# Optimization experiments

Measured on AMD Instinct MI355X. Metric: run time of the kernel, lower is better.

Reference implementation:

```python
import jax, jax.numpy as jnp
import numpy as np

B, TV, TH, F, H, D = 16, 128, 64, 512, 512, 256


def setup_inputs() -> dict:
    key = jax.random.key(0)
    ks = jax.random.split(key, 6)
    return {
        "v": jax.random.normal(ks[0], (B, TV, F), dtype=jnp.float32),
        "h": jax.random.normal(ks[1], (B, TH, H), dtype=jnp.float32),
        "W": jax.random.normal(ks[2], (F, D), dtype=jnp.float32) * 0.05,
        "U": jax.random.normal(ks[3], (H, D), dtype=jnp.float32) * 0.05,
        "b": jax.random.normal(ks[4], (D,), dtype=jnp.float32) * 0.05,
        "w": jax.random.normal(ks[5], (D, 1), dtype=jnp.float32) * 0.05,
    }


def reference(v, h, W, U, b, w):
    # v: [B, Tv, F] video features; h: [B, Th, H] decoder hidden states
    Wv = jnp.einsum("btf,fd->btd", v, W)      # [B, Tv, D]
    Uh = jnp.einsum("bsh,hd->bsd", h, U)      # [B, Th, D]
    # Broadcast add -> [B, Th, Tv, D], tanh nonlinearity (additive attention)
    f = jnp.tanh(Uh[:, :, None, :] + Wv[:, None, :, :] + b)
    q = jnp.einsum("bstd,d->bst", f, w[:, 0])  # scores [B, Th, Tv]
    beta = jax.nn.softmax(q, axis=-1)           # softmax over Tv (axis -2 of q[..., None])
    u = jnp.einsum("bst,btf->bsf", beta, v)    # context [B, Th, F]
    return u
```

## Files before the change

### kernel.cpp

```cpp
#include <hip/hip_runtime.h>
#include <hip/hip_bf16.h>

#define BB 16
#define TV 128
#define TH 64
#define FF 512
#define HH 512
#define DD 256

#define LOG2E2 2.8853900817779268f

typedef __attribute__((ext_vector_type(8))) short bf16x8;
typedef __attribute__((ext_vector_type(4))) float f32x4;

__device__ __forceinline__ float fast_exp2(float x) {
#if __has_builtin(__builtin_amdgcn_exp2f)
  return __builtin_amdgcn_exp2f(x);
#else
  return __expf(x * 0.6931471805599453f);
#endif
}
__device__ __forceinline__ float fast_rcp(float x) {
#if __has_builtin(__builtin_amdgcn_rcpf)
  return __builtin_amdgcn_rcpf(x);
#else
  return 1.0f / x;
#endif
}
__device__ __forceinline__ unsigned short f2bf(float x) {
  union { float f; unsigned u; } a; a.f = x;
  unsigned r = a.u + 0x7fffu + ((a.u >> 16) & 1u);
  return (unsigned short)(r >> 16);
}

#define NT_V 262144
#define NT_H 131072
#define NT_W 32768
__global__ __launch_bounds__(256) void convert_kernel(
    const float* __restrict__ v, const float* __restrict__ h,
    const float* __restrict__ W, const float* __restrict__ U,
    unsigned short* __restrict__ vb, unsigned short* __restrict__ hb,
    unsigned short* __restrict__ WT, unsigned short* __restrict__ UT) {
  int task = blockIdx.x * 256 + threadIdx.x;
  if (task < NT_V) {
    float4 x = ((const float4*)v)[task];
    ushort4 o = make_ushort4(f2bf(x.x), f2bf(x.y), f2bf(x.z), f2bf(x.w));
    *(ushort4*)&vb[(size_t)task * 4] = o;
  } else if (task < NT_V + NT_H) {
    int t2 = task - NT_V;
    float4 x = ((const float4*)h)[t2];
    ushort4 o = make_ushort4(f2bf(x.x), f2bf(x.y), f2bf(x.z), f2bf(x.w));
    *(ushort4*)&hb[(size_t)t2 * 4] = o;
  } else {
    int t2 = task - NT_V - NT_H;
    const float* S;
    unsigned short* Dt;
    if (t2 < NT_W) { S = W; Dt = WT; } else { S = U; Dt = UT; t2 -= NT_W; }
    int n = t2 & 255, k4 = t2 >> 8;
    float a0 = S[(k4 * 4 + 0) * 256 + n];
    float a1 = S[(k4 * 4 + 1) * 256 + n];
    float a2 = S[(k4 * 4 + 2) * 256 + n];
    float a3 = S[(k4 * 4 + 3) * 256 + n];
    ushort4 o = make_ushort4(f2bf(a0), f2bf(a1), f2bf(a2), f2bf(a3));
    *(ushort4*)&Dt[(size_t)n * 512 + k4 * 4] = o;
  }
}

__global__ __launch_bounds__(128) void mfma_gemm_kernel(
    const unsigned short* __restrict__ Av, const unsigned short* __restrict__ Ah,
    const unsigned short* __restrict__ WT, const unsigned short* __restrict__ UT,
    const float* __restrict__ bias, float* __restrict__ Wv2T,
    float* __restrict__ Uh2) {
  const int bid = blockIdx.x;
  const unsigned short* A;
  const unsigned short* BT;
  int mt, nt;
  bool is_wv;
  if (bid < 256) {
    A = Av; BT = WT; is_wv = true;
    mt = bid >> 3; nt = bid & 7;
  } else {
    const int b2 = bid - 256;
    A = Ah; BT = UT; is_wv = false;
    mt = b2 >> 3; nt = b2 & 7;
  }
  const int wv   = threadIdx.x >> 6;
  const int lane = threadIdx.x & 63;
  const int m0   = mt * 64 + wv * 32;
  const int n0   = nt * 32;
  const int r16  = lane & 15;
  const int quad = lane >> 4;

  const unsigned short* a0p = A + (size_t)(m0 + r16) * 512 + quad * 8;
  const unsigned short* a1p = a0p + 16 * 512;
  const unsigned short* b0p = BT + (size_t)(n0 + r16) * 512 + quad * 8;
  const unsigned short* b1p = b0p + 16 * 512;

  f32x4 acc00 = {0.f, 0.f, 0.f, 0.f};
  f32x4 acc01 = {0.f, 0.f, 0.f, 0.f};
  f32x4 acc10 = {0.f, 0.f, 0.f, 0.f};
  f32x4 acc11 = {0.f, 0.f, 0.f, 0.f};

#pragma unroll
  for (int kc = 0; kc < 16; kc++) {
    bf16x8 a0 = *(const bf16x8*)(a0p + kc * 32);
    bf16x8 a1 = *(const bf16x8*)(a1p + kc * 32);
    bf16x8 b0 = *(const bf16x8*)(b0p + kc * 32);
    bf16x8 b1 = *(const bf16x8*)(b1p + kc * 32);
    acc00 = __builtin_amdgcn_mfma_f32_16x16x32_bf16(a0, b0, acc00, 0, 0, 0);
    acc01 = __builtin_amdgcn_mfma_f32_16x16x32_bf16(a0, b1, acc01, 0, 0, 0);
    acc10 = __builtin_amdgcn_mfma_f32_16x16x32_bf16(a1, b0, acc10, 0, 0, 0);
    acc11 = __builtin_amdgcn_mfma_f32_16x16x32_bf16(a1, b1, acc11, 0, 0, 0);
  }

  if (is_wv) {
    const int bb   = m0 >> 7;
    const int tb   = (m0 & 127) + quad * 4;
    float* Wb = Wv2T + (size_t)bb * 32768;
#pragma unroll
    for (int r = 0; r < 4; r++) {
      Wb[(size_t)(n0 + r16) * 128 + tb + r]        = acc00[r] * LOG2E2;
      Wb[(size_t)(n0 + 16 + r16) * 128 + tb + r]   = acc01[r] * LOG2E2;
      Wb[(size_t)(n0 + r16) * 128 + tb + 16 + r]   = acc10[r] * LOG2E2;
      Wb[(size_t)(n0 + 16 + r16) * 128 + tb + 16 + r] = acc11[r] * LOG2E2;
    }
  } else {
    const float bj0 = bias[n0 + r16];
    const float bj1 = bias[n0 + 16 + r16];
#pragma unroll
    for (int r = 0; r < 4; r++) {
      const int row0 = m0 + quad * 4 + r;
      Uh2[(size_t)row0 * 256 + n0 + r16]             = (acc00[r] + bj0) * LOG2E2;
      Uh2[(size_t)row0 * 256 + n0 + 16 + r16]        = (acc01[r] + bj1) * LOG2E2;
      Uh2[(size_t)(row0 + 16) * 256 + n0 + r16]      = (acc10[r] + bj0) * LOG2E2;
      Uh2[(size_t)(row0 + 16) * 256 + n0 + 16 + r16] = (acc11[r] + bj1) * LOG2E2;
    }
  }
}

__global__ __launch_bounds__(1024) void attn_fused_kernel(
    const float* __restrict__ Wv2T, const float* __restrict__ Uh2,
    const float* __restrict__ wg, const float* __restrict__ v,
    float* __restrict__ u) {
  __shared__ float UhS[4 * 256];
  __shared__ float wS[256];
  __shared__ float pS[4 * 1024];
  __shared__ float bS[4 * 128];
  __shared__ float mW[8];
  __shared__ float sW[8];

  const int tid = threadIdx.x;
  const int b   = blockIdx.x >> 4;
  const int sg  = blockIdx.x & 15;
  const int s0  = sg * 4;

  if (tid < 256) {
    const int row = tid >> 6, q4 = (tid & 63) << 2;
    *(float4*)&UhS[row * 256 + q4] =
        *(const float4*)&Uh2[(size_t)(b * 64 + s0 + row) * 256 + q4];
  } else if (tid < 320) {
    const int q4 = (tid - 256) << 2;
    *(float4*)&wS[q4] = *(const float4*)&wg[q4];
  }
  __syncthreads();

  {
    const int t4 = tid & 31;
    const int dg = (tid >> 5) & 7;
    const int s  = tid >> 8;
    const float* wvb = Wv2T + (size_t)b * 32768 + (size_t)dg * 32 * 128 + t4 * 4;
    const float* uhp = &UhS[s * 256 + dg * 32];
    const float* wp  = &wS[dg * 32];
    float4 acc = {0.f, 0.f, 0.f, 0.f};
#pragma unroll 8
    for (int j = 0; j < 32; j++) {
      float4 a  = *(const float4*)(wvb + j * 128);
      float uh = uhp[j];
      float ww = wp[j];
      acc.x = fmaf(ww, fast_rcp(fast_exp2(a.x + uh) + 1.0f), acc.x);
      acc.y = fmaf(ww, fast_rcp(fast_exp2(a.y + uh) + 1.0f), acc.y);
      acc.z = fmaf(ww, fast_rcp(fast_exp2(a.z + uh) + 1.0f), acc.z);
      acc.w = fmaf(ww, fast_rcp(fast_exp2(a.w + uh) + 1.0f), acc.w);
    }
    *(float4*)&pS[s * 1024 + dg * 128 + t4 * 4] = acc;
  }
  __syncthreads();

  float qv = 0.0f, ev = 0.0f;
  const int wvid = tid >> 6, lane = tid & 63;
  if (tid < 512) {
    const int s_l = tid >> 7, t = tid & 127;
    float ssum = 0.0f;
#pragma unroll
    for (int dg = 0; dg < 8; dg++) ssum += pS[s_l * 1024 + dg * 128 + t];
    qv = ssum * (-LOG2E2);
    float m = qv;
#pragma unroll
    for (int off = 32; off > 0; off >>= 1) m = fmaxf(m, __shfl_xor(m, off, 64));
    if (lane == 0) mW[wvid] = m;
  }
  __syncthreads();
  if (tid < 512) {
    float m = fmaxf(mW[wvid], mW[wvid ^ 1]);
    ev = fast_exp2(qv - m);
    float ssum = ev;
#pragma unroll
    for (int off = 32; off > 0; off >>= 1) ssum += __shfl_xor(ssum, off, 64);
    if (lane == 0) sW[wvid] = ssum;
  }
  __syncthreads();
  if (tid < 512) {
    const int s_l = tid >> 7, t = tid & 127;
    bS[s_l * 128 + t] = ev * fast_rcp(sW[wvid] + sW[wvid ^ 1]);
  }
  __syncthreads();

  const float* vb2 = v + (size_t)b * TV * FF;
  const int f  = tid & 511;
  const int sh = tid >> 9;
  float a0 = 0.f, a1 = 0.f;
#pragma unroll 4
  for (int tg = 0; tg < 128; tg += 4) {
    float4 b0 = *(const float4*)&bS[(sh * 2 + 0) * 128 + tg];
    float4 b1 = *(const float4*)&bS[(sh * 2 + 1) * 128 + tg];
    float v0 = vb2[(tg + 0) * 512 + f];
    float v1 = vb2[(tg + 1) * 512 + f];
    float v2 = vb2[(tg + 2) * 512 + f];
    float v3 = vb2[(tg + 3) * 512 + f];
    a0 = fmaf(b0.x, v0, a0); a0 = fmaf(b0.y, v1, a0);
    a0 = fmaf(b0.z, v2, a0); a0 = fmaf(b0.w, v3, a0);
    a1 = fmaf(b1.x, v0, a1); a1 = fmaf(b1.y, v1, a1);
    a1 = fmaf(b1.z, v2, a1); a1 = fmaf(b1.w, v3, a1);
  }
  float* urow = u + (size_t)(b * 64 + s0 + sh * 2) * 512;
  urow[0 * 512 + f] = a0;
  urow[1 * 512 + f] = a1;
}

extern "C" void kernel_launch(void* const* d_in, const int* in_sizes, int n_in,
                              void* d_out, int out_size, void* d_ws, size_t ws_size,
                              hipStream_t stream) {
  const float* v  = (const float*)d_in[0];
  const float* h  = (const float*)d_in[1];
  const float* W  = (const float*)d_in[2];
  const float* U  = (const float*)d_in[3];
  const float* bb = (const float*)d_in[4];
  const float* w  = (const float*)d_in[5];
  float* u = (float*)d_out;

  float* Wv2T = (float*)d_ws;
  float* Uh2  = Wv2T + (size_t)2048 * 256;
  unsigned short* vb16 = (unsigned short*)(Uh2 + (size_t)1024 * 256);
  unsigned short* hb16 = vb16 + (size_t)2048 * 512;
  unsigned short* WT   = hb16 + (size_t)1024 * 512;
  unsigned short* UT   = WT + (size_t)256 * 512;

  convert_kernel<<<1792, 256, 0, stream>>>(v, h, W, U, vb16, hb16, WT, UT);
  mfma_gemm_kernel<<<384, 128, 0, stream>>>(vb16, hb16, WT, UT, bb, Wv2T, Uh2);
  attn_fused_kernel<<<256, 1024, 0, stream>>>(Wv2T, Uh2, w, v, u);
}
```

Baseline: 92.87 us.

## Rebalance GEMM and attention grids, read bf16 video features in context sum

The GEMM now uses 256-thread blocks covering 128 rows each, so it launches half as many blocks, and the Wv transposed output is written as float4 stores instead of scalar ones. The attention kernel drops to 512 threads handling 2 query rows per block and runs 512 blocks, which gives more blocks for the same work. It also reads the bf16 copy of v in the final weighted sum, halving the bytes read there. The risks are that each v element is now reloaded by twice as many blocks, and that using bf16 v in the context sum adds rounding error to the output.

```diff
diff --git a/kernel.cpp b/kernel.cpp
--- a/kernel.cpp
+++ b/kernel.cpp
@@ -31,6 +31,10 @@
   union { float f; unsigned u; } a; a.f = x;
   unsigned r = a.u + 0x7fffu + ((a.u >> 16) & 1u);
   return (unsigned short)(r >> 16);
+}
+__device__ __forceinline__ float bf2f(unsigned short x) {
+  union { unsigned u; float f; } a; a.u = ((unsigned)x) << 16;
+  return a.f;
 }
 
 #define NT_V 262144
@@ -66,7 +70,7 @@
   }
 }
 
-__global__ __launch_bounds__(128) void mfma_gemm_kernel(
+__global__ __launch_bounds__(256) void mfma_gemm_kernel(
     const unsigned short* __restrict__ Av, const unsigned short* __restrict__ Ah,
     const unsigned short* __restrict__ WT, const unsigned short* __restrict__ UT,
     const float* __restrict__ bias, float* __restrict__ Wv2T,
@@ -76,17 +80,17 @@
   const unsigned short* BT;
   int mt, nt;
   bool is_wv;
-  if (bid < 256) {
+  if (bid < 128) {
     A = Av; BT = WT; is_wv = true;
     mt = bid >> 3; nt = bid & 7;
   } else {
-    const int b2 = bid - 256;
+    const int b2 = bid - 128;
     A = Ah; BT = UT; is_wv = false;
     mt = b2 >> 3; nt = b2 & 7;
   }
   const int wv   = threadIdx.x >> 6;
   const int lane = threadIdx.x & 63;
-  const int m0   = mt * 64 + wv * 32;
+  const int m0   = mt * 128 + wv * 32;
   const int n0   = nt * 32;
   const int r16  = lane & 15;
   const int quad = lane >> 4;
@@ -101,7 +105,7 @@
   f32x4 acc10 = {0.f, 0.f, 0.f, 0.f};
   f32x4 acc11 = {0.f, 0.f, 0.f, 0.f};
 
-#pragma unroll
+#pragma unroll 4
   for (int kc = 0; kc < 16; kc++) {
     bf16x8 a0 = *(const bf16x8*)(a0p + kc * 32);
     bf16x8 a1 = *(const bf16x8*)(a1p + kc * 32);
@@ -114,16 +118,20 @@
   }
 
   if (is_wv) {
-    const int bb   = m0 >> 7;
-    const int tb   = (m0 & 127) + quad * 4;
-    float* Wb = Wv2T + (size_t)bb * 32768;
+    const int tb = (m0 & 127) + quad * 4;
+    float* Wb = Wv2T + (size_t)mt * 32768;
+    float4 s00, s01, s10, s11;
 #pragma unroll
     for (int r = 0; r < 4; r++) {
-      Wb[(size_t)(n0 + r16) * 128 + tb + r]        = acc00[r] * LOG2E2;
-      Wb[(size_t)(n0 + 16 + r16) * 128 + tb + r]   = acc01[r] * LOG2E2;
-      Wb[(size_t)(n0 + r16) * 128 + tb + 16 + r]   = acc10[r] * LOG2E2;
-      Wb[(size_t)(n0 + 16 + r16) * 128 + tb + 16 + r] = acc11[r] * LOG2E2;
+      (&s00.x)[r] = acc00[r] * LOG2E2;
+      (&s01.x)[r] = acc01[r] * LOG2E2;
+      (&s10.x)[r] = acc10[r] * LOG2E2;
+      (&s11.x)[r] = acc11[r] * LOG2E2;
     }
+    *(float4*)&Wb[(size_t)(n0 + r16) * 128 + tb]           = s00;
+    *(float4*)&Wb[(size_t)(n0 + r16) * 128 + tb + 16]      = s10;
+    *(float4*)&Wb[(size_t)(n0 + 16 + r16) * 128 + tb]      = s01;
+    *(float4*)&Wb[(size_t)(n0 + 16 + r16) * 128 + tb + 16] = s11;
   } else {
     const float bj0 = bias[n0 + r16];
     const float bj1 = bias[n0 + 16 + r16];
@@ -138,28 +146,28 @@
   }
 }
 
-__global__ __launch_bounds__(1024) void attn_fused_kernel(
+__global__ __launch_bounds__(512) void attn_fused_kernel(
     const float* __restrict__ Wv2T, const float* __restrict__ Uh2,
-    const float* __restrict__ wg, const float* __restrict__ v,
+    const float* __restrict__ wg, const unsigned short* __restrict__ vb16,
     float* __restrict__ u) {
-  __shared__ float UhS[4 * 256];
+  __shared__ float UhS[2 * 256];
   __shared__ float wS[256];
-  __shared__ float pS[4 * 1024];
-  __shared__ float bS[4 * 128];
-  __shared__ float mW[8];
-  __shared__ float sW[8];
+  __shared__ float pS[8 * 2 * 128];
+  __shared__ float bS[2 * 128];
+  __shared__ float mW[4];
+  __shared__ float sW[4];
 
   const int tid = threadIdx.x;
-  const int b   = blockIdx.x >> 4;
-  const int sg  = blockIdx.x & 15;
-  const int s0  = sg * 4;
-
-  if (tid < 256) {
+  const int b   = blockIdx.x >> 5;
+  const int sg  = blockIdx.x & 31;
+  const int s0  = sg * 2;
+
+  if (tid < 128) {
     const int row = tid >> 6, q4 = (tid & 63) << 2;
     *(float4*)&UhS[row * 256 + q4] =
         *(const float4*)&Uh2[(size_t)(b * 64 + s0 + row) * 256 + q4];
-  } else if (tid < 320) {
-    const int q4 = (tid - 256) << 2;
+  } else if (tid < 192) {
+    const int q4 = (tid - 128) << 2;
     *(float4*)&wS[q4] = *(const float4*)&wg[q4];
   }
   __syncthreads();
@@ -169,30 +177,35 @@
     const int dg = (tid >> 5) & 7;
     const int s  = tid >> 8;
     const float* wvb = Wv2T + (size_t)b * 32768 + (size_t)dg * 32 * 128 + t4 * 4;
-    const float* uhp = &UhS[s * 256 + dg * 32];
-    const float* wp  = &wS[dg * 32];
+    const float4* uhq = (const float4*)&UhS[s * 256 + dg * 32];
+    const float4* wq  = (const float4*)&wS[dg * 32];
     float4 acc = {0.f, 0.f, 0.f, 0.f};
-#pragma unroll 8
-    for (int j = 0; j < 32; j++) {
-      float4 a  = *(const float4*)(wvb + j * 128);
-      float uh = uhp[j];
-      float ww = wp[j];
-      acc.x = fmaf(ww, fast_rcp(fast_exp2(a.x + uh) + 1.0f), acc.x);
-      acc.y = fmaf(ww, fast_rcp(fast_exp2(a.y + uh) + 1.0f), acc.y);
-      acc.z = fmaf(ww, fast_rcp(fast_exp2(a.z + uh) + 1.0f), acc.z);
-      acc.w = fmaf(ww, fast_rcp(fast_exp2(a.w + uh) + 1.0f), acc.w);
+#pragma unroll
+    for (int jq = 0; jq < 8; jq++) {
+      float4 uh4 = uhq[jq];
+      float4 w4  = wq[jq];
+#pragma unroll
+      for (int jj = 0; jj < 4; jj++) {
+        float4 a  = *(const float4*)(wvb + (jq * 4 + jj) * 128);
+        float uh = (&uh4.x)[jj];
+        float ww = (&w4.x)[jj];
+        acc.x = fmaf(ww, fast_rcp(fast_exp2(a.x + uh) + 1.0f), acc.x);
+        acc.y = fmaf(ww, fast_rcp(fast_exp2(a.y + uh) + 1.0f), acc.y);
+        acc.z = fmaf(ww, fast_rcp(fast_exp2(a.z + uh) + 1.0f), acc.z);
+        acc.w = fmaf(ww, fast_rcp(fast_exp2(a.w + uh) + 1.0f), acc.w);
+      }
     }
-    *(float4*)&pS[s * 1024 + dg * 128 + t4 * 4] = acc;
+    *(float4*)&pS[(dg * 2 + s) * 128 + t4 * 4] = acc;
   }
   __syncthreads();
 
   float qv = 0.0f, ev = 0.0f;
   const int wvid = tid >> 6, lane = tid & 63;
-  if (tid < 512) {
+  if (tid < 256) {
     const int s_l = tid >> 7, t = tid & 127;
     float ssum = 0.0f;
 #pragma unroll
-    for (int dg = 0; dg < 8; dg++) ssum += pS[s_l * 1024 + dg * 128 + t];
+    for (int dg = 0; dg < 8; dg++) ssum += pS[(dg * 2 + s_l) * 128 + t];
     qv = ssum * (-LOG2E2);
     float m = qv;
 #pragma unroll
@@ -200,7 +213,7 @@
     if (lane == 0) mW[wvid] = m;
   }
   __syncthreads();
-  if (tid < 512) {
+  if (tid < 256) {
     float m = fmaxf(mW[wvid], mW[wvid ^ 1]);
     ev = fast_exp2(qv - m);
     float ssum = ev;
@@ -209,30 +222,29 @@
     if (lane == 0) sW[wvid] = ssum;
   }
   __syncthreads();
-  if (tid < 512) {
+  if (tid < 256) {
     const int s_l = tid >> 7, t = tid & 127;
     bS[s_l * 128 + t] = ev * fast_rcp(sW[wvid] + sW[wvid ^ 1]);
   }
   __syncthreads();
 
-  const float* vb2 = v + (size_t)b * TV * FF;
-  const int f  = tid & 511;
-  const int sh = tid >> 9;
+  const unsigned short* vb2 = vb16 + (size_t)b * TV * FF;
+  const int f = tid;
   float a0 = 0.f, a1 = 0.f;
 #pragma unroll 4
   for (int tg = 0; tg < 128; tg += 4) {
-    float4 b0 = *(const float4*)&bS[(sh * 2 + 0) * 128 + tg];
-    float4 b1 = *(const float4*)&bS[(sh * 2 + 1) * 128 + tg];
-    float v0 = vb2[(tg + 0) * 512 + f];
-    float v1 = vb2[(tg + 1) * 512 + f];
-    float v2 = vb2[(tg + 2) * 512 + f];
-    float v3 = vb2[(tg + 3) * 512 + f];
+    float4 b0 = *(const float4*)&bS[0 * 128 + tg];
+    float4 b1 = *(const float4*)&bS[1 * 128 + tg];
+    float v0 = bf2f(vb2[(tg + 0) * 512 + f]);
+    float v1 = bf2f(vb2[(tg + 1) * 512 + f]);
+    float v2 = bf2f(vb2[(tg + 2) * 512 + f]);
+    float v3 = bf2f(vb2[(tg + 3) * 512 + f]);
     a0 = fmaf(b0.x, v0, a0); a0 = fmaf(b0.y, v1, a0);
     a0 = fmaf(b0.z, v2, a0); a0 = fmaf(b0.w, v3, a0);
     a1 = fmaf(b1.x, v0, a1); a1 = fmaf(b1.y, v1, a1);
     a1 = fmaf(b1.z, v2, a1); a1 = fmaf(b1.w, v3, a1);
   }
-  float* urow = u + (size_t)(b * 64 + s0 + sh * 2) * 512;
+  float* urow = u + (size_t)(b * 64 + s0) * 512;
   urow[0 * 512 + f] = a0;
   urow[1 * 512 + f] = a1;
 }
@@ -256,6 +268,6 @@
   unsigned short* UT   = WT + (size_t)256 * 512;
 
   convert_kernel<<<1792, 256, 0, stream>>>(v, h, W, U, vb16, hb16, WT, UT);
-  mfma_gemm_kernel<<<384, 128, 0, stream>>>(vb16, hb16, WT, UT, bb, Wv2T, Uh2);
-  attn_fused_kernel<<<256, 1024, 0, stream>>>(Wv2T, Uh2, w, v, u);
-}
+  mfma_gemm_kernel<<<192, 256, 0, stream>>>(vb16, hb16, WT, UT, bb, Wv2T, Uh2);
+  attn_fused_kernel<<<512, 512, 0, stream>>>(Wv2T, Uh2, w, vb16, u);
+}
```

Result: slower. 97.97 us (+5.5%).

## Reuse each Wv load across four Th rows and vectorize Wv2T stores

Applied to the files above, without the earlier changes.

The score stage now has each thread load one Wv column chunk and apply it to all four Th rows in the block, with the 256-wide D axis split into 32 groups of 8 instead of 4 rows times 8 groups of 32. This cuts global loads of Wv2T per block by four and raises per-thread ILP. The cost is a larger shared partial-sum buffer (64KB) and a 32-term reduction instead of 8. Separately, the projection kernel writes Wv2T with float4 stores instead of scalar stores.

```diff
diff --git a/kernel.cpp b/kernel.cpp
--- a/kernel.cpp
+++ b/kernel.cpp
@@ -114,16 +114,21 @@
   }
 
   if (is_wv) {
-    const int bb   = m0 >> 7;
-    const int tb   = (m0 & 127) + quad * 4;
+    const int bb = m0 >> 7;
+    const int tb = (m0 & 127) + quad * 4;
     float* Wb = Wv2T + (size_t)bb * 32768;
+    float4 s00, s01, s10, s11;
 #pragma unroll
     for (int r = 0; r < 4; r++) {
-      Wb[(size_t)(n0 + r16) * 128 + tb + r]        = acc00[r] * LOG2E2;
-      Wb[(size_t)(n0 + 16 + r16) * 128 + tb + r]   = acc01[r] * LOG2E2;
-      Wb[(size_t)(n0 + r16) * 128 + tb + 16 + r]   = acc10[r] * LOG2E2;
-      Wb[(size_t)(n0 + 16 + r16) * 128 + tb + 16 + r] = acc11[r] * LOG2E2;
+      (&s00.x)[r] = acc00[r] * LOG2E2;
+      (&s01.x)[r] = acc01[r] * LOG2E2;
+      (&s10.x)[r] = acc10[r] * LOG2E2;
+      (&s11.x)[r] = acc11[r] * LOG2E2;
     }
+    *(float4*)&Wb[(size_t)(n0 + r16) * 128 + tb]           = s00;
+    *(float4*)&Wb[(size_t)(n0 + r16) * 128 + tb + 16]      = s10;
+    *(float4*)&Wb[(size_t)(n0 + 16 + r16) * 128 + tb]      = s01;
+    *(float4*)&Wb[(size_t)(n0 + 16 + r16) * 128 + tb + 16] = s11;
   } else {
     const float bj0 = bias[n0 + r16];
     const float bj1 = bias[n0 + 16 + r16];
@@ -144,7 +149,7 @@
     float* __restrict__ u) {
   __shared__ float UhS[4 * 256];
   __shared__ float wS[256];
-  __shared__ float pS[4 * 1024];
+  __shared__ float pS[32 * 4 * 128];
   __shared__ float bS[4 * 128];
   __shared__ float mW[8];
   __shared__ float sW[8];
@@ -166,23 +171,41 @@
 
   {
     const int t4 = tid & 31;
-    const int dg = (tid >> 5) & 7;
-    const int s  = tid >> 8;
-    const float* wvb = Wv2T + (size_t)b * 32768 + (size_t)dg * 32 * 128 + t4 * 4;
-    const float* uhp = &UhS[s * 256 + dg * 32];
-    const float* wp  = &wS[dg * 32];
-    float4 acc = {0.f, 0.f, 0.f, 0.f};
-#pragma unroll 8
-    for (int j = 0; j < 32; j++) {
+    const int dg = tid >> 5;
+    const float* wvb = Wv2T + (size_t)b * 32768 + (size_t)dg * 8 * 128 + t4 * 4;
+    float4 acc0 = {0.f, 0.f, 0.f, 0.f};
+    float4 acc1 = {0.f, 0.f, 0.f, 0.f};
+    float4 acc2 = {0.f, 0.f, 0.f, 0.f};
+    float4 acc3 = {0.f, 0.f, 0.f, 0.f};
+#pragma unroll
+    for (int j = 0; j < 8; j++) {
       float4 a  = *(const float4*)(wvb + j * 128);
-      float uh = uhp[j];
-      float ww = wp[j];
-      acc.x = fmaf(ww, fast_rcp(fast_exp2(a.x + uh) + 1.0f), acc.x);
-      acc.y = fmaf(ww, fast_rcp(fast_exp2(a.y + uh) + 1.0f), acc.y);
-      acc.z = fmaf(ww, fast_rcp(fast_exp2(a.z + uh) + 1.0f), acc.z);
-      acc.w = fmaf(ww, fast_rcp(fast_exp2(a.w + uh) + 1.0f), acc.w);
+      float ww  = wS[dg * 8 + j];
+      float uh0 = UhS[0 * 256 + dg * 8 + j];
+      float uh1 = UhS[1 * 256 + dg * 8 + j];
+      float uh2 = UhS[2 * 256 + dg * 8 + j];
+      float uh3 = UhS[3 * 256 + dg * 8 + j];
+      acc0.x = fmaf(ww, fast_rcp(fast_exp2(a.x + uh0) + 1.0f), acc0.x);
+      acc0.y = fmaf(ww, fast_rcp(fast_exp2(a.y + uh0) + 1.0f), acc0.y);
+      acc0.z = fmaf(ww, fast_rcp(fast_exp2(a.z + uh0) + 1.0f), acc0.z);
+      acc0.w = fmaf(ww, fast_rcp(fast_exp2(a.w + uh0) + 1.0f), acc0.w);
+      acc1.x = fmaf(ww, fast_rcp(fast_exp2(a.x + uh1) + 1.0f), acc1.x);
+      acc1.y = fmaf(ww, fast_rcp(fast_exp2(a.y + uh1) + 1.0f), acc1.y);
+      acc1.z = fmaf(ww, fast_rcp(fast_exp2(a.z + uh1) + 1.0f), acc1.z);
+      acc1.w = fmaf(ww, fast_rcp(fast_exp2(a.w + uh1) + 1.0f), acc1.w);
+      acc2.x = fmaf(ww, fast_rcp(fast_exp2(a.x + uh2) + 1.0f), acc2.x);
+      acc2.y = fmaf(ww, fast_rcp(fast_exp2(a.y + uh2) + 1.0f), acc2.y);
+      acc2.z = fmaf(ww, fast_rcp(fast_exp2(a.z + uh2) + 1.0f), acc2.z);
+      acc2.w = fmaf(ww, fast_rcp(fast_exp2(a.w + uh2) + 1.0f), acc2.w);
+      acc3.x = fmaf(ww, fast_rcp(fast_exp2(a.x + uh3) + 1.0f), acc3.x);
+      acc3.y = fmaf(ww, fast_rcp(fast_exp2(a.y + uh3) + 1.0f), acc3.y);
+      acc3.z = fmaf(ww, fast_rcp(fast_exp2(a.z + uh3) + 1.0f), acc3.z);
+      acc3.w = fmaf(ww, fast_rcp(fast_exp2(a.w + uh3) + 1.0f), acc3.w);
     }
-    *(float4*)&pS[s * 1024 + dg * 128 + t4 * 4] = acc;
+    *(float4*)&pS[(dg * 4 + 0) * 128 + t4 * 4] = acc0;
+    *(float4*)&pS[(dg * 4 + 1) * 128 + t4 * 4] = acc1;
+    *(float4*)&pS[(dg * 4 + 2) * 128 + t4 * 4] = acc2;
+    *(float4*)&pS[(dg * 4 + 3) * 128 + t4 * 4] = acc3;
   }
   __syncthreads();
 
@@ -192,7 +215,7 @@
     const int s_l = tid >> 7, t = tid & 127;
     float ssum = 0.0f;
 #pragma unroll
-    for (int dg = 0; dg < 8; dg++) ssum += pS[s_l * 1024 + dg * 128 + t];
+    for (int dg = 0; dg < 32; dg++) ssum += pS[(dg * 4 + s_l) * 128 + t];
     qv = ssum * (-LOG2E2);
     float m = qv;
 #pragma unroll
```

After: 96.87 us. +4.3%, slower.
